# Kernel tuning notes

Hardware: AMD Instinct MI355X
Metric: run time of the kernel (lower is better)

The kernel has to match this reference:

```python
import jax, jax.numpy as jnp
import numpy as np

B, H, O = 16384, 1024, 512


def setup_inputs() -> dict:
    key = jax.random.key(0)
    ks = jax.random.split(key, 8)
    s = 1.0 / np.sqrt(H)  # PyTorch-style uniform init scale (values only matter for numerics)
    return {
        "inp": jax.random.normal(ks[0], (B, O), jnp.float32),
        "hidden": jax.random.normal(ks[1], (1, B, H), jnp.float32),
        "w_ih": jax.random.uniform(ks[2], (3 * H, O), jnp.float32, -s, s),
        "w_hh": jax.random.uniform(ks[3], (3 * H, H), jnp.float32, -s, s),
        "b_ih": jax.random.uniform(ks[4], (3 * H,), jnp.float32, -s, s),
        "b_hh": jax.random.uniform(ks[5], (3 * H,), jnp.float32, -s, s),
        "w_out": jax.random.uniform(ks[6], (O, H), jnp.float32, -s, s),
        "b_out": jax.random.uniform(ks[7], (O,), jnp.float32, -s, s),
    }


def reference(inp, hidden, w_ih, w_hh, b_ih, b_hh, w_out, b_out):
    # Single-step GRU (PyTorch gate order r, z, n) + Linear + tanh.
    h = hidden[0]                                # [B, H]
    gi = inp @ w_ih.T + b_ih                     # [B, 3H]
    gh = h @ w_hh.T + b_hh                       # [B, 3H]
    i_r, i_z, i_n = jnp.split(gi, 3, axis=-1)
    h_r, h_z, h_n = jnp.split(gh, 3, axis=-1)
    r = jax.nn.sigmoid(i_r + h_r)
    z = jax.nn.sigmoid(i_z + h_z)
    n = jnp.tanh(i_n + r * h_n)
    h_new = (1.0 - z) * n + z * h                # [B, H]
    out = jnp.tanh(h_new @ w_out.T + b_out)      # [B, O]
    return out, h_new[None]                      # hidden back to [1, B, H]
```

## Files before the change

### kernel.cpp

```cpp
#include <hip/hip_runtime.h>

typedef __bf16 bf16x8 __attribute__((ext_vector_type(8)));
typedef float  f32x4  __attribute__((ext_vector_type(4)));
typedef unsigned short us8 __attribute__((ext_vector_type(8)));

__device__ __forceinline__ unsigned short f2bf(float f) {
  unsigned int u = __builtin_bit_cast(unsigned int, f);
  u += 0x7FFFu + ((u >> 16) & 1u);
  return (unsigned short)(u >> 16);
}
__device__ __forceinline__ float sigmoid_f(float x) {
  return 1.f / (1.f + __expf(-x));
}
__device__ __forceinline__ float tanh_f(float x) {
  float e = __expf(2.f * x);
  return 1.f - 2.f / (e + 1.f);
}

__global__ void cast_f32_bf16(const float* __restrict__ in,
                              unsigned short* __restrict__ out, long n) {
  long i = ((long)blockIdx.x * blockDim.x + threadIdx.x) * 8;
  if (i >= n) return;
  f32x4 a = *(const f32x4*)(in + i);
  f32x4 b = *(const f32x4*)(in + i + 4);
  us8 o;
  o[0] = f2bf(a[0]); o[1] = f2bf(a[1]); o[2] = f2bf(a[2]); o[3] = f2bf(a[3]);
  o[4] = f2bf(b[0]); o[5] = f2bf(b[1]); o[6] = f2bf(b[2]); o[7] = f2bf(b[3]);
  *(us8*)(out + i) = o;
}

__device__ __forceinline__ void relayout_region(
    const float* __restrict__ srcRowBase, size_t rowStride,
    unsigned short* __restrict__ dst, float* __restrict__ lp, int lane) {
  {
    int r = lane >> 2, c = (lane & 3) << 3;
    const float* s = srcRowBase + (size_t)r * rowStride + c;
    f32x4 a = *(const f32x4*)(s);
    f32x4 b = *(const f32x4*)(s + 4);
#pragma unroll
    for (int j = 0; j < 4; ++j) { lp[r * 33 + c + j] = a[j]; lp[r * 33 + c + 4 + j] = b[j]; }
  }
  int s4 = lane >> 4, r16 = lane & 15;
  us8 o;
#pragma unroll
  for (int j = 0; j < 8; ++j) o[j] = f2bf(lp[r16 * 33 + s4 * 8 + j]);
  *(us8*)(dst + lane * 8) = o;
}

__global__ __launch_bounds__(256) void relayout_A(
    const float* __restrict__ src, unsigned short* __restrict__ dst, int K) {
  __shared__ float lp[4][16 * 33];
  const int wIn = threadIdx.x >> 6, lane = threadIdx.x & 63;
  const int gw  = blockIdx.x * 4 + wIn;
  const int nkt = K >> 5;
  const int p = gw / nkt, kt = gw - p * nkt;
  const float* base = src + (size_t)p * 128 * K + kt * 32;
  unsigned short* d = dst + (size_t)gw * 4096;
#pragma unroll
  for (int g = 0; g < 8; ++g)
    relayout_region(base + (size_t)g * 16 * K, K, d + g * 512, lp[wIn], lane);
}

__global__ __launch_bounds__(256) void relayout_W(
    const float* __restrict__ src, unsigned short* __restrict__ dst, int K) {
  __shared__ float lp[4][16 * 33];
  const int wIn = threadIdx.x >> 6, lane = threadIdx.x & 63;
  const int gw  = blockIdx.x * 4 + wIn;
  const int nkt = K >> 5;
  const int qg = gw / nkt, kt = gw - qg * nkt;
  const int q = qg / 3, g = qg - q * 3;
  const float* base = src + ((size_t)g * 1024 + q * 64) * K + kt * 32;
  unsigned short* d = dst + (size_t)gw * 2048;
#pragma unroll
  for (int rg = 0; rg < 4; ++rg)
    relayout_region(base + (size_t)rg * 16 * K, K, d + rg * 512, lp[wIn], lane);
}

#define GLOAD(gp, lp) __builtin_amdgcn_global_load_lds( \
    (const __attribute__((address_space(1))) unsigned int*)(gp), \
    (__attribute__((address_space(3))) unsigned int*)(lp), 16, 0, 0)

__global__ __launch_bounds__(256, 2) void fused_gru(
    const unsigned short* __restrict__ inp_r,
    const unsigned short* __restrict__ h_r,
    const unsigned short* __restrict__ wih_r,
    const unsigned short* __restrict__ whh_r,
    const float* __restrict__ b_ih,
    const float* __restrict__ b_hh,
    const float* __restrict__ hidden,
    float* __restrict__ hnew_f32,
    unsigned short* __restrict__ hnew_b)
{
  __shared__ unsigned short ls[4][10240];

  const int tid  = threadIdx.x;
  const int lane = tid & 63;
  const int wave = tid >> 6;
  const int wr = wave >> 1, wc = wave & 1;

  f32x4 accR[4][2], accZ[4][2], accNi[4][2], accNh[4][2];
#pragma unroll
  for (int m = 0; m < 4; ++m)
#pragma unroll
    for (int n = 0; n < 2; ++n) {
      accR[m][n]  = f32x4{0.f, 0.f, 0.f, 0.f};
      accZ[m][n]  = f32x4{0.f, 0.f, 0.f, 0.f};
      accNi[m][n] = f32x4{0.f, 0.f, 0.f, 0.f};
      accNh[m][n] = f32x4{0.f, 0.f, 0.f, 0.f};
    }

  const int t4   = lane >> 4;
  const int l15  = lane & 15;
  const int rofs = t4 * 128 + l15 * 8;

  const unsigned short* aptr = inp_r + (size_t)blockIdx.y * (16 * 4096);
  const unsigned short* wptr = wih_r + (size_t)blockIdx.x * (3 * 16 * 2048);
  int wgs = 16 * 2048;

#define STAGE(BUF) do { \
    GLOAD(aptr + tid * 8,           &ls[BUF][tid * 8]); \
    GLOAD(aptr + 2048 + tid * 8,    &ls[BUF][2048 + tid * 8]); \
    GLOAD(wptr + tid * 8,           &ls[BUF][4096 + tid * 8]); \
    GLOAD(wptr + wgs + tid * 8,     &ls[BUF][6144 + tid * 8]); \
    GLOAD(wptr + 2 * wgs + tid * 8, &ls[BUF][8192 + tid * 8]); \
    aptr += 4096; wptr += 2048; \
  } while (0)

#define COMPUTE(BUF, ACCN) do { \
    const unsigned short* lb = &ls[BUF][0]; \
    bf16x8 af[4], bfr[3][2]; \
    _Pragma("unroll") for (int m = 0; m < 4; ++m) \
      af[m] = *(const bf16x8*)&lb[(wr * 4 + m) * 512 + rofs]; \
    _Pragma("unroll") for (int g = 0; g < 3; ++g) { \
      _Pragma("unroll") for (int n = 0; n < 2; ++n) \
        bfr[g][n] = *(const bf16x8*)&lb[4096 + g * 2048 + (wc * 2 + n) * 512 + rofs]; \
    } \
    __builtin_amdgcn_s_setprio(1); \
    _Pragma("unroll") for (int m = 0; m < 4; ++m) { \
      _Pragma("unroll") for (int n = 0; n < 2; ++n) { \
        accR[m][n] = __builtin_amdgcn_mfma_f32_16x16x32_bf16(af[m], bfr[0][n], accR[m][n], 0, 0, 0); \
        accZ[m][n] = __builtin_amdgcn_mfma_f32_16x16x32_bf16(af[m], bfr[1][n], accZ[m][n], 0, 0, 0); \
        ACCN[m][n] = __builtin_amdgcn_mfma_f32_16x16x32_bf16(af[m], bfr[2][n], ACCN[m][n], 0, 0, 0); \
      } \
    } \
    __builtin_amdgcn_s_setprio(0); \
  } while (0)

#define WAIT10 asm volatile("s_waitcnt vmcnt(10)" ::: "memory")
#define BARR   __builtin_amdgcn_s_barrier()
#define STEP(SB, CB, ACCN) do { STAGE(SB); WAIT10; BARR; COMPUTE(CB, ACCN); } while (0)

  STAGE(0); STAGE(1);
#pragma unroll 1
  for (int i = 0; i < 3; ++i) {
    STEP(2, 0, accNi); STEP(3, 1, accNi); STEP(0, 2, accNi); STEP(1, 3, accNi);
  }
  STEP(2, 0, accNi);
  STEP(3, 1, accNi);
  aptr = h_r + (size_t)blockIdx.y * (32 * 4096);
  wptr = whh_r + (size_t)blockIdx.x * (3 * 32 * 2048);
  wgs = 32 * 2048;
  STEP(0, 2, accNi);
  STEP(1, 3, accNi);
#pragma unroll 1
  for (int i = 0; i < 7; ++i) {
    STEP(2, 0, accNh); STEP(3, 1, accNh); STEP(0, 2, accNh); STEP(1, 3, accNh);
  }
  STEP(2, 0, accNh);
  STEP(3, 1, accNh);
  asm volatile("s_waitcnt vmcnt(5)" ::: "memory"); BARR;
  COMPUTE(2, accNh);
  asm volatile("s_waitcnt vmcnt(0)" ::: "memory"); BARR;
  COMPUTE(3, accNh);

#undef STAGE
#undef COMPUTE
#undef WAIT10
#undef BARR
#undef STEP

  const int m0 = blockIdx.y * 128;
  const int n0 = blockIdx.x * 64;
  const int colb = n0 + wc * 32 + l15;
  const int rowb = m0 + wr * 64 + (t4 << 2);
#pragma unroll
  for (int n = 0; n < 2; ++n) {
    int c = colb + n * 16;
    float br  = b_ih[c]        + b_hh[c];
    float bz  = b_ih[1024 + c] + b_hh[1024 + c];
    float bni = b_ih[2048 + c];
    float bnh = b_hh[2048 + c];
#pragma unroll
    for (int m = 0; m < 4; ++m) {
      int row = rowb + m * 16;
#pragma unroll
      for (int r = 0; r < 4; ++r) {
        float rg = sigmoid_f(accR[m][n][r] + br);
        float zg = sigmoid_f(accZ[m][n][r] + bz);
        float ng = tanh_f((accNi[m][n][r] + bni) + rg * (accNh[m][n][r] + bnh));
        float ho = hidden[(size_t)(row + r) * 1024 + c];
        float hv = (1.f - zg) * ng + zg * ho;
        hnew_f32[(size_t)(row + r) * 1024 + c] = hv;
        hnew_b [(size_t)(row + r) * 1024 + c] = f2bf(hv);
      }
    }
  }
}

__global__ __launch_bounds__(256) void gemm_out(
    const unsigned short* __restrict__ A,
    const unsigned short* __restrict__ Bm,
    float* __restrict__ Cout,
    const float* __restrict__ bias,
    int M, int N, int K)
{
  __shared__ unsigned short lsA[2][128 * 32];
  __shared__ unsigned short lsB[2][128 * 32];

  const int tid  = threadIdx.x;
  const int lane = tid & 63;
  const int wave = tid >> 6;
  const int wr = wave >> 1, wc = wave & 1;
  const int m0 = blockIdx.y * 128;
  const int n0 = blockIdx.x * 128;

  auto stage = [&](int buf, int kt) {
    const int k0 = kt * 32;
#pragma unroll
    for (int it = 0; it < 2; ++it) {
      int li  = it * 256 + tid;
      int row = li >> 2;
      int col = (li & 3) << 3;
      GLOAD(A  + (size_t)(m0 + row) * K + k0 + col, &lsA[buf][li * 8]);
      GLOAD(Bm + (size_t)(n0 + row) * K + k0 + col, &lsB[buf][li * 8]);
    }
  };

  f32x4 acc[4][4];
#pragma unroll
  for (int i = 0; i < 4; ++i)
#pragma unroll
    for (int j = 0; j < 4; ++j) acc[i][j] = f32x4{0.f, 0.f, 0.f, 0.f};

  const int nk = K >> 5;
  stage(0, 0);
  int buf = 0;
  for (int kt = 0; kt < nk; ++kt) {
    if (kt + 1 < nk) {
      stage(buf ^ 1, kt + 1);
      asm volatile("s_waitcnt vmcnt(4)" ::: "memory");
    } else {
      asm volatile("s_waitcnt vmcnt(0)" ::: "memory");
    }
    __builtin_amdgcn_s_barrier();
    const int kofs = (lane >> 4) << 3;
    const int rA = wr * 64 + (lane & 15);
    const int rB = wc * 64 + (lane & 15);
    bf16x8 af[4], bfr[4];
#pragma unroll
    for (int m = 0; m < 4; ++m)
      af[m] = *(const bf16x8*)&lsA[buf][(rA + m * 16) * 32 + kofs];
#pragma unroll
    for (int n = 0; n < 4; ++n)
      bfr[n] = *(const bf16x8*)&lsB[buf][(rB + n * 16) * 32 + kofs];
#pragma unroll
    for (int m = 0; m < 4; ++m)
#pragma unroll
      for (int n = 0; n < 4; ++n)
        acc[m][n] = __builtin_amdgcn_mfma_f32_16x16x32_bf16(af[m], bfr[n], acc[m][n], 0, 0, 0);
    __builtin_amdgcn_s_barrier();
    buf ^= 1;
  }

  const int colb = n0 + wc * 64 + (lane & 15);
  const int rowb = m0 + wr * 64 + ((lane >> 4) << 2);
#pragma unroll
  for (int n = 0; n < 4; ++n) {
    int col = colb + n * 16;
    float bv = bias[col];
#pragma unroll
    for (int m = 0; m < 4; ++m) {
      int row = rowb + m * 16;
#pragma unroll
      for (int r = 0; r < 4; ++r) {
        Cout[(size_t)(row + r) * N + col] = tanh_f(acc[m][n][r] + bv);
      }
    }
  }
}

extern "C" void kernel_launch(void* const* d_in, const int* in_sizes, int n_in,
                              void* d_out, int out_size, void* d_ws, size_t ws_size,
                              hipStream_t stream) {
  const int B = 16384, H = 1024, O = 512;
  const float* inp    = (const float*)d_in[0];
  const float* hidden = (const float*)d_in[1];
  const float* w_ih   = (const float*)d_in[2];
  const float* w_hh   = (const float*)d_in[3];
  const float* b_ih   = (const float*)d_in[4];
  const float* b_hh   = (const float*)d_in[5];
  const float* w_out  = (const float*)d_in[6];
  const float* b_out  = (const float*)d_in[7];

  float* out      = (float*)d_out;
  float* hnew_out = out + (size_t)B * O;

  char* ws = (char*)d_ws;
  size_t need = 0;
  auto carve = [&](size_t elems) {
    unsigned short* p = (unsigned short*)(ws + need);
    need += elems * 2;
    return p;
  };
  unsigned short* inp_r  = carve((size_t)B * O);
  unsigned short* h_r    = carve((size_t)B * H);
  unsigned short* wih_r  = carve((size_t)3 * H * O);
  unsigned short* whh_r  = carve((size_t)3 * H * H);
  unsigned short* wout_b = carve((size_t)O * H);
  unsigned short* hnew_b = carve((size_t)B * H);
  if (ws_size < need) return;

  relayout_A<<<dim3((B / 128) * (O / 32) / 4), dim3(256), 0, stream>>>(inp, inp_r, O);
  relayout_A<<<dim3((B / 128) * (H / 32) / 4), dim3(256), 0, stream>>>(hidden, h_r, H);
  relayout_W<<<dim3((H / 64) * 3 * (O / 32) / 4), dim3(256), 0, stream>>>(w_ih, wih_r, O);
  relayout_W<<<dim3((H / 64) * 3 * (H / 32) / 4), dim3(256), 0, stream>>>(w_hh, whh_r, H);
  cast_f32_bf16<<<dim3((unsigned)(((size_t)O * H / 8 + 255) / 256)), dim3(256), 0, stream>>>(
      w_out, wout_b, (long)O * H);

  fused_gru<<<dim3(H / 64, B / 128), dim3(256), 0, stream>>>(
      inp_r, h_r, wih_r, whh_r, b_ih, b_hh, hidden, hnew_out, hnew_b);

  gemm_out<<<dim3(O / 128, B / 128), dim3(256), 0, stream>>>(
      hnew_b, wout_b, out, b_out, B, O, H);
}
```

Baseline: 235.9 us.

## Merge prep kernels and feed output GEMM from pre-tiled images with 4-stage pipeline

Merges the five relayout and cast launches into one prep_all kernel, which also tiles w_out into the MFMA-friendly image layout. fused_gru now writes the bf16 h_new directly in that tiled layout, so gemm_out loads contiguous 8 KB tiles with a 4-buffer global_load_lds pipeline, priority hints around the MFMAs, and 2 blocks per CU. The goal is to cut launch overhead and strided loads in the output GEMM. In exchange, fused_gru's bf16 stores become scattered, and gemm_out is hardcoded to K=1024 and N=512.

```diff
diff --git a/kernel.cpp b/kernel.cpp
--- a/kernel.cpp
+++ b/kernel.cpp
@@ -15,18 +15,6 @@
 __device__ __forceinline__ float tanh_f(float x) {
   float e = __expf(2.f * x);
   return 1.f - 2.f / (e + 1.f);
-}
-
-__global__ void cast_f32_bf16(const float* __restrict__ in,
-                              unsigned short* __restrict__ out, long n) {
-  long i = ((long)blockIdx.x * blockDim.x + threadIdx.x) * 8;
-  if (i >= n) return;
-  f32x4 a = *(const f32x4*)(in + i);
-  f32x4 b = *(const f32x4*)(in + i + 4);
-  us8 o;
-  o[0] = f2bf(a[0]); o[1] = f2bf(a[1]); o[2] = f2bf(a[2]); o[3] = f2bf(a[3]);
-  o[4] = f2bf(b[0]); o[5] = f2bf(b[1]); o[6] = f2bf(b[2]); o[7] = f2bf(b[3]);
-  *(us8*)(out + i) = o;
 }
 
 __device__ __forceinline__ void relayout_region(
@@ -47,33 +35,42 @@
   *(us8*)(dst + lane * 8) = o;
 }
 
-__global__ __launch_bounds__(256) void relayout_A(
-    const float* __restrict__ src, unsigned short* __restrict__ dst, int K) {
+__global__ __launch_bounds__(256) void prep_all(
+    const float* __restrict__ inp, const float* __restrict__ hidden,
+    const float* __restrict__ w_ih, const float* __restrict__ w_hh,
+    const float* __restrict__ w_out,
+    unsigned short* __restrict__ inp_r, unsigned short* __restrict__ h_r,
+    unsigned short* __restrict__ wih_r, unsigned short* __restrict__ whh_r,
+    unsigned short* __restrict__ wout_r)
+{
   __shared__ float lp[4][16 * 33];
   const int wIn = threadIdx.x >> 6, lane = threadIdx.x & 63;
   const int gw  = blockIdx.x * 4 + wIn;
+
+  const float* src; unsigned short* dst; int K, local, isA;
+  if      (gw < 2048) { src = inp;    dst = inp_r;  K = 512;  isA = 1; local = gw; }
+  else if (gw < 6144) { src = hidden; dst = h_r;    K = 1024; isA = 1; local = gw - 2048; }
+  else if (gw < 6912) { src = w_ih;   dst = wih_r;  K = 512;  isA = 0; local = gw - 6144; }
+  else if (gw < 8448) { src = w_hh;   dst = whh_r;  K = 1024; isA = 0; local = gw - 6912; }
+  else                { src = w_out;  dst = wout_r; K = 1024; isA = 1; local = gw - 8448; }
   const int nkt = K >> 5;
-  const int p = gw / nkt, kt = gw - p * nkt;
-  const float* base = src + (size_t)p * 128 * K + kt * 32;
-  unsigned short* d = dst + (size_t)gw * 4096;
-#pragma unroll
-  for (int g = 0; g < 8; ++g)
-    relayout_region(base + (size_t)g * 16 * K, K, d + g * 512, lp[wIn], lane);
-}
-
-__global__ __launch_bounds__(256) void relayout_W(
-    const float* __restrict__ src, unsigned short* __restrict__ dst, int K) {
-  __shared__ float lp[4][16 * 33];
-  const int wIn = threadIdx.x >> 6, lane = threadIdx.x & 63;
-  const int gw  = blockIdx.x * 4 + wIn;
-  const int nkt = K >> 5;
-  const int qg = gw / nkt, kt = gw - qg * nkt;
-  const int q = qg / 3, g = qg - q * 3;
-  const float* base = src + ((size_t)g * 1024 + q * 64) * K + kt * 32;
-  unsigned short* d = dst + (size_t)gw * 2048;
-#pragma unroll
-  for (int rg = 0; rg < 4; ++rg)
-    relayout_region(base + (size_t)rg * 16 * K, K, d + rg * 512, lp[wIn], lane);
+
+  if (isA) {
+    int p = local / nkt, kt = local - p * nkt;
+    const float* base = src + (size_t)p * 128 * K + kt * 32;
+    unsigned short* d = dst + (size_t)local * 4096;
+#pragma unroll
+    for (int g = 0; g < 8; ++g)
+      relayout_region(base + (size_t)g * 16 * K, K, d + g * 512, lp[wIn], lane);
+  } else {
+    int qg = local / nkt, kt = local - qg * nkt;
+    int q = qg / 3, g = qg - q * 3;
+    const float* base = src + ((size_t)g * 1024 + q * 64) * K + kt * 32;
+    unsigned short* d = dst + (size_t)local * 2048;
+#pragma unroll
+    for (int rg = 0; rg < 4; ++rg)
+      relayout_region(base + (size_t)rg * 16 * K, K, d + rg * 512, lp[wIn], lane);
+  }
 }
 
 #define GLOAD(gp, lp) __builtin_amdgcn_global_load_lds( \
@@ -89,7 +86,7 @@
     const float* __restrict__ b_hh,
     const float* __restrict__ hidden,
     float* __restrict__ hnew_f32,
-    unsigned short* __restrict__ hnew_b)
+    unsigned short* __restrict__ hnew_img)
 {
   __shared__ unsigned short ls[4][10240];
 
@@ -190,6 +187,9 @@
     float bz  = b_ih[1024 + c] + b_hh[1024 + c];
     float bni = b_ih[2048 + c];
     float bnh = b_hh[2048 + c];
+    const int kt = c >> 5;
+    const int s  = (c >> 3) & 3;
+    const int e  = c & 7;
 #pragma unroll
     for (int m = 0; m < 4; ++m) {
       int row = rowb + m * 16;
@@ -198,82 +198,93 @@
         float rg = sigmoid_f(accR[m][n][r] + br);
         float zg = sigmoid_f(accZ[m][n][r] + bz);
         float ng = tanh_f((accNi[m][n][r] + bni) + rg * (accNh[m][n][r] + bnh));
-        float ho = hidden[(size_t)(row + r) * 1024 + c];
+        int rw = row + r;
+        float ho = hidden[(size_t)rw * 1024 + c];
         float hv = (1.f - zg) * ng + zg * ho;
-        hnew_f32[(size_t)(row + r) * 1024 + c] = hv;
-        hnew_b [(size_t)(row + r) * 1024 + c] = f2bf(hv);
+        hnew_f32[(size_t)rw * 1024 + c] = hv;
+        size_t img = ((size_t)((rw >> 7) * 32 + kt)) * 4096
+                   + (((rw >> 4) & 7) * 512) + s * 128 + (rw & 15) * 8 + e;
+        hnew_img[img] = f2bf(hv);
       }
     }
   }
 }
 
-__global__ __launch_bounds__(256) void gemm_out(
-    const unsigned short* __restrict__ A,
-    const unsigned short* __restrict__ Bm,
+__global__ __launch_bounds__(256, 2) void gemm_out(
+    const unsigned short* __restrict__ A_img,
+    const unsigned short* __restrict__ B_img,
     float* __restrict__ Cout,
-    const float* __restrict__ bias,
-    int M, int N, int K)
+    const float* __restrict__ bias)
 {
-  __shared__ unsigned short lsA[2][128 * 32];
-  __shared__ unsigned short lsB[2][128 * 32];
+  __shared__ unsigned short ls[4][8192];
 
   const int tid  = threadIdx.x;
   const int lane = tid & 63;
   const int wave = tid >> 6;
   const int wr = wave >> 1, wc = wave & 1;
+
+  f32x4 acc[4][4];
+#pragma unroll
+  for (int i = 0; i < 4; ++i)
+#pragma unroll
+    for (int j = 0; j < 4; ++j) acc[i][j] = f32x4{0.f, 0.f, 0.f, 0.f};
+
+  const int t4   = lane >> 4;
+  const int l15  = lane & 15;
+  const int rofs = t4 * 128 + l15 * 8;
+
+  const unsigned short* aptr = A_img + (size_t)blockIdx.y * (32 * 4096);
+  const unsigned short* bptr = B_img + (size_t)blockIdx.x * (32 * 4096);
+
+#define STAGE(BUF) do { \
+    GLOAD(aptr + tid * 8,        &ls[BUF][tid * 8]); \
+    GLOAD(aptr + 2048 + tid * 8, &ls[BUF][2048 + tid * 8]); \
+    GLOAD(bptr + tid * 8,        &ls[BUF][4096 + tid * 8]); \
+    GLOAD(bptr + 2048 + tid * 8, &ls[BUF][6144 + tid * 8]); \
+    aptr += 4096; bptr += 4096; \
+  } while (0)
+
+#define COMPUTE(BUF) do { \
+    const unsigned short* lb = &ls[BUF][0]; \
+    bf16x8 af[4], bfr[4]; \
+    _Pragma("unroll") for (int m = 0; m < 4; ++m) \
+      af[m] = *(const bf16x8*)&lb[(wr * 4 + m) * 512 + rofs]; \
+    _Pragma("unroll") for (int n = 0; n < 4; ++n) \
+      bfr[n] = *(const bf16x8*)&lb[4096 + (wc * 4 + n) * 512 + rofs]; \
+    __builtin_amdgcn_s_setprio(1); \
+    _Pragma("unroll") for (int m = 0; m < 4; ++m) { \
+      _Pragma("unroll") for (int n = 0; n < 4; ++n) \
+        acc[m][n] = __builtin_amdgcn_mfma_f32_16x16x32_bf16(af[m], bfr[n], acc[m][n], 0, 0, 0); \
+    } \
+    __builtin_amdgcn_s_setprio(0); \
+  } while (0)
+
+#define WAIT8 asm volatile("s_waitcnt vmcnt(8)" ::: "memory")
+#define BARR  __builtin_amdgcn_s_barrier()
+#define STEP(SB, CB) do { STAGE(SB); WAIT8; BARR; COMPUTE(CB); } while (0)
+
+  STAGE(0); STAGE(1);
+#pragma unroll 1
+  for (int i = 0; i < 7; ++i) {
+    STEP(2, 0); STEP(3, 1); STEP(0, 2); STEP(1, 3);
+  }
+  STEP(2, 0);
+  STEP(3, 1);
+  asm volatile("s_waitcnt vmcnt(4)" ::: "memory"); BARR;
+  COMPUTE(2);
+  asm volatile("s_waitcnt vmcnt(0)" ::: "memory"); BARR;
+  COMPUTE(3);
+
+#undef STAGE
+#undef COMPUTE
+#undef WAIT8
+#undef BARR
+#undef STEP
+
   const int m0 = blockIdx.y * 128;
   const int n0 = blockIdx.x * 128;
-
-  auto stage = [&](int buf, int kt) {
-    const int k0 = kt * 32;
-#pragma unroll
-    for (int it = 0; it < 2; ++it) {
-      int li  = it * 256 + tid;
-      int row = li >> 2;
-      int col = (li & 3) << 3;
-      GLOAD(A  + (size_t)(m0 + row) * K + k0 + col, &lsA[buf][li * 8]);
-      GLOAD(Bm + (size_t)(n0 + row) * K + k0 + col, &lsB[buf][li * 8]);
-    }
-  };
-
-  f32x4 acc[4][4];
-#pragma unroll
-  for (int i = 0; i < 4; ++i)
-#pragma unroll
-    for (int j = 0; j < 4; ++j) acc[i][j] = f32x4{0.f, 0.f, 0.f, 0.f};
-
-  const int nk = K >> 5;
-  stage(0, 0);
-  int buf = 0;
-  for (int kt = 0; kt < nk; ++kt) {
-    if (kt + 1 < nk) {
-      stage(buf ^ 1, kt + 1);
-      asm volatile("s_waitcnt vmcnt(4)" ::: "memory");
-    } else {
-      asm volatile("s_waitcnt vmcnt(0)" ::: "memory");
-    }
-    __builtin_amdgcn_s_barrier();
-    const int kofs = (lane >> 4) << 3;
-    const int rA = wr * 64 + (lane & 15);
-    const int rB = wc * 64 + (lane & 15);
-    bf16x8 af[4], bfr[4];
-#pragma unroll
-    for (int m = 0; m < 4; ++m)
-      af[m] = *(const bf16x8*)&lsA[buf][(rA + m * 16) * 32 + kofs];
-#pragma unroll
-    for (int n = 0; n < 4; ++n)
-      bfr[n] = *(const bf16x8*)&lsB[buf][(rB + n * 16) * 32 + kofs];
-#pragma unroll
-    for (int m = 0; m < 4; ++m)
-#pragma unroll
-      for (int n = 0; n < 4; ++n)
-        acc[m][n] = __builtin_amdgcn_mfma_f32_16x16x32_bf16(af[m], bfr[n], acc[m][n], 0, 0, 0);
-    __builtin_amdgcn_s_barrier();
-    buf ^= 1;
-  }
-
-  const int colb = n0 + wc * 64 + (lane & 15);
-  const int rowb = m0 + wr * 64 + ((lane >> 4) << 2);
+  const int colb = n0 + wc * 64 + l15;
+  const int rowb = m0 + wr * 64 + (t4 << 2);
 #pragma unroll
   for (int n = 0; n < 4; ++n) {
     int col = colb + n * 16;
@@ -283,7 +294,7 @@
       int row = rowb + m * 16;
 #pragma unroll
       for (int r = 0; r < 4; ++r) {
-        Cout[(size_t)(row + r) * N + col] = tanh_f(acc[m][n][r] + bv);
+        Cout[(size_t)(row + r) * 512 + col] = tanh_f(acc[m][n][r] + bv);
       }
     }
   }
@@ -316,20 +327,16 @@
   unsigned short* h_r    = carve((size_t)B * H);
   unsigned short* wih_r  = carve((size_t)3 * H * O);
   unsigned short* whh_r  = carve((size_t)3 * H * H);
-  unsigned short* wout_b = carve((size_t)O * H);
-  unsigned short* hnew_b = carve((size_t)B * H);
+  unsigned short* wout_r = carve((size_t)O * H);
+  unsigned short* hnew_i = carve((size_t)B * H);
   if (ws_size < need) return;
 
-  relayout_A<<<dim3((B / 128) * (O / 32) / 4), dim3(256), 0, stream>>>(inp, inp_r, O);
-  relayout_A<<<dim3((B / 128) * (H / 32) / 4), dim3(256), 0, stream>>>(hidden, h_r, H);
-  relayout_W<<<dim3((H / 64) * 3 * (O / 32) / 4), dim3(256), 0, stream>>>(w_ih, wih_r, O);
-  relayout_W<<<dim3((H / 64) * 3 * (H / 32) / 4), dim3(256), 0, stream>>>(w_hh, whh_r, H);
-  cast_f32_bf16<<<dim3((unsigned)(((size_t)O * H / 8 + 255) / 256)), dim3(256), 0, stream>>>(
-      w_out, wout_b, (long)O * H);
+  prep_all<<<dim3(2144), dim3(256), 0, stream>>>(
+      inp, hidden, w_ih, w_hh, w_out, inp_r, h_r, wih_r, whh_r, wout_r);
 
   fused_gru<<<dim3(H / 64, B / 128), dim3(256), 0, stream>>>(
-      inp_r, h_r, wih_r, whh_r, b_ih, b_hh, hidden, hnew_out, hnew_b);
+      inp_r, h_r, wih_r, whh_r, b_ih, b_hh, hidden, hnew_out, hnew_i);
 
   gemm_out<<<dim3(O / 128, B / 128), dim3(256), 0, stream>>>(
-      hnew_b, wout_b, out, b_out, B, O, H);
-}
+      hnew_i, wout_r, out, b_out);
+}
```

Result: faster. 220.0 us (-6.8%).
